# Optimization experiments

Measured on AMD Instinct MI355X. Metric: run time of the kernel, lower is better.

The kernel has to match this reference:

```python
import jax, jax.numpy as jnp
import numpy as np

B, N, F, K = 512, 512, 512, 10
D = F // 2

def setup_inputs() -> dict:
    key = jax.random.key(0)
    k1, k2, k3 = jax.random.split(key, 3)
    ins_emb = jax.random.normal(k1, (B, N, F), dtype=jnp.float32)
    attn = jax.random.uniform(k2, (B, N, 1), dtype=jnp.float32)
    # xavier_uniform for a (D, D) linear weight
    limit = float(np.sqrt(6.0 / (D + D)))
    W = jax.random.uniform(k3, (D, D), dtype=jnp.float32, minval=-limit, maxval=limit)
    return {"ins_emb": ins_emb, "attn": attn, "W": W}

def reference(ins_emb, attn, W):
    d = ins_emb.shape[-1] // 2
    drug = ins_emb[:, :, :d]          # [B, N, d]
    dis = ins_emb[:, :, d:]           # [B, N, d]
    # torch Linear: drug @ W^T, then per-instance dot with dis -> scalar
    proj = jnp.einsum('bnd,ed->bne', drug, W)          # [B, N, d]
    pred = jnp.sum(proj * dis, axis=-1, keepdims=True) # [B, N, 1]
    attn_pred = attn * pred                            # [B, N, 1]
    topk_vals, _ = jax.lax.top_k(attn_pred[:, :, 0], K)  # [B, K]
    return jnp.mean(topk_vals, axis=1, keepdims=True)    # [B, 1]
```

## Files before the change

### kernel.cpp

```cpp
#include <hip/hip_runtime.h>
#include <hip/hip_bf16.h>
#include <cstdint>

#define BB 512
#define NN 512
#define FF 512
#define DD 256
#define KTOP 10
#define BM 32
#define GRID 256
#define TPB 32

typedef __attribute__((ext_vector_type(8))) short bf16x8;
typedef __attribute__((ext_vector_type(4))) float f32x4;

__device__ __forceinline__ ushort f2bf(float x){
  union { __hip_bfloat16 h; ushort u; } cv;
  cv.h = __float2bfloat16(x);
  return cv.u;
}

__device__ __forceinline__ bf16x8 cvt8(f32x4 a, f32x4 b){
  bf16x8 r;
  r[0]=(short)f2bf(a[0]); r[1]=(short)f2bf(a[1]); r[2]=(short)f2bf(a[2]); r[3]=(short)f2bf(a[3]);
  r[4]=(short)f2bf(b[0]); r[5]=(short)f2bf(b[1]); r[6]=(short)f2bf(b[2]); r[7]=(short)f2bf(b[3]);
  return r;
}

#define GL2LDS(GSRC, LDST)                                                          \
  __builtin_amdgcn_global_load_lds(                                                 \
      (const __attribute__((address_space(1))) uint32_t*)(uintptr_t)(GSRC),         \
      (__attribute__((address_space(3))) uint32_t*)(uint32_t)(uintptr_t)(LDST),     \
      16, 0, 0)

__global__ __launch_bounds__(512, 2)
void fused_kernel(const float* __restrict__ emb, const float* __restrict__ attn,
                  const float* __restrict__ W, float* __restrict__ out){
  __shared__ float LA[BM*FF];
  __shared__ float LB[BM*FF];
  __shared__ float red[2][8][BM];
  __shared__ float attn_l[TPB*BM];
  __shared__ float scores_l[TPB*BM];

  const int tid  = threadIdx.x;
  const int w    = tid >> 6;
  const int lane = tid & 63;
  const int g    = lane >> 4;
  const int c    = lane & 15;
  const int s    = w & 3;
  const int h    = w >> 2;

  int offs[8];
#pragma unroll
  for (int i = 0; i < 8; ++i){
    int idx = w*8 + i;
    int r = idx >> 1, hf = idx & 1;
    offs[i] = r*FF + hf*256 + ((lane ^ (r & 7)) << 2);
  }
  const float* tbase = emb + (size_t)blockIdx.x * (TPB*BM*FF);

#pragma unroll
  for (int i = 0; i < 8; ++i)
    GL2LDS(tbase + offs[i], &LA[(w*8 + i)*256]);

  attn_l[tid]       = attn[blockIdx.x*(TPB*BM) + tid];
  attn_l[tid + 512] = attn[blockIdx.x*(TPB*BM) + 512 + tid];

  bf16x8 Wf[4][4];
#pragma unroll
  for (int eb = 0; eb < 4; ++eb)
#pragma unroll
    for (int kb = 0; kb < 4; ++kb){
      const float* wp = W + (s*64 + eb*16 + c)*DD + h*128 + kb*32 + g*8;
      f32x4 q0 = *reinterpret_cast<const f32x4*>(wp);
      f32x4 q1 = *reinterpret_cast<const f32x4*>(wp + 4);
      Wf[eb][kb] = cvt8(q0, q1);
    }

  __syncthreads();

#define TILE_BODY(T, RD, WR, PAR)                                                   \
  do {                                                                              \
    if ((T) + 1 < TPB){                                                             \
      const float* nb_ = tbase + (size_t)((T)+1) * (BM*FF);                         \
      _Pragma("unroll")                                                             \
      for (int i = 0; i < 8; ++i)                                                   \
        GL2LDS(nb_ + offs[i], &WR[(w*8 + i)*256]);                                  \
    }                                                                               \
    const f32x4* Lv = (const f32x4*)&RD[0];                                         \
    _Pragma("unroll")                                                               \
    for (int mb = 0; mb < 2; ++mb){                                                 \
      const int m0 = mb*16;                                                         \
      const int rb = (m0 + c)*128;                                                  \
      const int x  = c & 7;                                                         \
      bf16x8 af[4];                                                                 \
      _Pragma("unroll")                                                             \
      for (int kb = 0; kb < 4; ++kb){                                               \
        int ch0 = h*32 + kb*8 + g*2;                                                \
        f32x4 q0 = Lv[rb + ((ch0    ) ^ x)];                                        \
        f32x4 q1 = Lv[rb + ((ch0 + 1) ^ x)];                                        \
        af[kb] = cvt8(q0, q1);                                                      \
      }                                                                             \
      float rs0=0.f, rs1=0.f, rs2=0.f, rs3=0.f;                                     \
      _Pragma("unroll")                                                             \
      for (int eb = 0; eb < 4; ++eb){                                               \
        f32x4 acc = {0.f, 0.f, 0.f, 0.f};                                           \
        _Pragma("unroll")                                                           \
        for (int kb = 0; kb < 4; ++kb)                                              \
          acc = __builtin_amdgcn_mfma_f32_16x16x32_bf16(af[kb], Wf[eb][kb], acc, 0, 0, 0); \
        const int sb = 64 + s*16 + eb*4 + (c >> 2);                                 \
        const int e3 = c & 3;                                                       \
        _Pragma("unroll")                                                           \
        for (int j = 0; j < 4; ++j){                                                \
          const int row = m0 + g*4 + j;                                             \
          const int fi  = row*FF + ((sb ^ (row & 7)) << 2) + e3;                    \
          float d = RD[fi];                                                         \
          if      (j == 0) rs0 += acc[0]*d;                                         \
          else if (j == 1) rs1 += acc[1]*d;                                         \
          else if (j == 2) rs2 += acc[2]*d;                                         \
          else             rs3 += acc[3]*d;                                         \
        }                                                                           \
      }                                                                             \
      rs0 += __shfl_xor(rs0,1); rs0 += __shfl_xor(rs0,2); rs0 += __shfl_xor(rs0,4); rs0 += __shfl_xor(rs0,8); \
      rs1 += __shfl_xor(rs1,1); rs1 += __shfl_xor(rs1,2); rs1 += __shfl_xor(rs1,4); rs1 += __shfl_xor(rs1,8); \
      rs2 += __shfl_xor(rs2,1); rs2 += __shfl_xor(rs2,2); rs2 += __shfl_xor(rs2,4); rs2 += __shfl_xor(rs2,8); \
      rs3 += __shfl_xor(rs3,1); rs3 += __shfl_xor(rs3,2); rs3 += __shfl_xor(rs3,4); rs3 += __shfl_xor(rs3,8); \
      if (c == 0){                                                                  \
        red[PAR][w][m0 + g*4 + 0] = rs0;                                            \
        red[PAR][w][m0 + g*4 + 1] = rs1;                                            \
        red[PAR][w][m0 + g*4 + 2] = rs2;                                            \
        red[PAR][w][m0 + g*4 + 3] = rs3;                                            \
      }                                                                             \
    }                                                                               \
    __syncthreads();                       \
    if (tid < BM){                                                                  \
      float sum = red[PAR][0][tid] + red[PAR][1][tid] + red[PAR][2][tid] + red[PAR][3][tid] \
                + red[PAR][4][tid] + red[PAR][5][tid] + red[PAR][6][tid] + red[PAR][7][tid]; \
      scores_l[(T)*BM + tid] = attn_l[(T)*BM + tid] * sum;                          \
    }                                                                               \
  } while(0)

  for (int t = 0; t < TPB; t += 2){
    TILE_BODY(t,     LA, LB, 0);
    TILE_BODY(t + 1, LB, LA, 1);
  }
#undef TILE_BODY

  __syncthreads();

  if (w < 2){
    const float* sc = scores_l + w*NN;
    float v0,v1,v2,v3,v4,v5,v6,v7;
    v0=sc[lane];     v1=sc[64+lane];  v2=sc[128+lane]; v3=sc[192+lane];
    v4=sc[256+lane]; v5=sc[320+lane]; v6=sc[384+lane]; v7=sc[448+lane];
    float total = 0.f;
    for (int it = 0; it < KTOP; ++it){
      float m = v0; int mj = 0;
      if (v1>m){m=v1;mj=1;} if (v2>m){m=v2;mj=2;} if (v3>m){m=v3;mj=3;}
      if (v4>m){m=v4;mj=4;} if (v5>m){m=v5;mj=5;} if (v6>m){m=v6;mj=6;}
      if (v7>m){m=v7;mj=7;}
      float bm = m; int bl = lane;
#pragma unroll
      for (int off = 32; off; off >>= 1){
        float om = __shfl_xor(bm, off);
        int   ol = __shfl_xor(bl, off);
        if (om > bm || (om == bm && ol < bl)){ bm = om; bl = ol; }
      }
      total += bm;
      if (lane == bl){
        if (mj==0) v0=-3.0e38f; else if (mj==1) v1=-3.0e38f;
        else if (mj==2) v2=-3.0e38f; else if (mj==3) v3=-3.0e38f;
        else if (mj==4) v4=-3.0e38f; else if (mj==5) v5=-3.0e38f;
        else if (mj==6) v6=-3.0e38f; else v7=-3.0e38f;
      }
    }
    if (lane == 0) out[blockIdx.x*2 + w] = total * (1.0f / KTOP);
  }
}

extern "C" void kernel_launch(void* const* d_in, const int* in_sizes, int n_in,
                              void* d_out, int out_size, void* d_ws, size_t ws_size,
                              hipStream_t stream){
  const float* emb  = (const float*)d_in[0];
  const float* attn = (const float*)d_in[1];
  const float* W    = (const float*)d_in[2];
  float* out = (float*)d_out;

  fused_kernel<<<GRID, 512, 0, stream>>>(emb, attn, W, out);
}
```

Before: 107.6 us.

## Use one 256-thread block per batch with 16-row tiles over 512 blocks

The kernel now launches 512 blocks of 256 threads, one per batch element, instead of 256 blocks of 512 threads that each covered two batches. Tiles shrink to 16 rows, and each wave handles 8 output column blocks, holding W fragments for 128 output columns in registers. The goal is to double the number of blocks so more CUs are busy and to halve LDS per block so more blocks fit per CU. The cost is twice the W-fragment registers per thread, which puts pressure on occupancy, and a barrier every 16 rows instead of every 32.

```diff
diff --git a/kernel.cpp b/kernel.cpp
--- a/kernel.cpp
+++ b/kernel.cpp
@@ -7,8 +7,8 @@
 #define FF 512
 #define DD 256
 #define KTOP 10
-#define BM 32
-#define GRID 256
+#define BM 16
+#define GRID 512
 #define TPB 32
 
 typedef __attribute__((ext_vector_type(8))) short bf16x8;
@@ -33,22 +33,22 @@
       (__attribute__((address_space(3))) uint32_t*)(uint32_t)(uintptr_t)(LDST),     \
       16, 0, 0)
 
-__global__ __launch_bounds__(512, 2)
+__global__ __launch_bounds__(256, 2)
 void fused_kernel(const float* __restrict__ emb, const float* __restrict__ attn,
                   const float* __restrict__ W, float* __restrict__ out){
   __shared__ float LA[BM*FF];
   __shared__ float LB[BM*FF];
-  __shared__ float red[2][8][BM];
-  __shared__ float attn_l[TPB*BM];
-  __shared__ float scores_l[TPB*BM];
+  __shared__ float red[2][4][BM];
+  __shared__ float attn_l[NN];
+  __shared__ float scores_l[NN];
 
   const int tid  = threadIdx.x;
   const int w    = tid >> 6;
   const int lane = tid & 63;
   const int g    = lane >> 4;
   const int c    = lane & 15;
-  const int s    = w & 3;
-  const int h    = w >> 2;
+  const int s    = w & 1;
+  const int h    = w >> 1;
 
   int offs[8];
 #pragma unroll
@@ -57,21 +57,21 @@
     int r = idx >> 1, hf = idx & 1;
     offs[i] = r*FF + hf*256 + ((lane ^ (r & 7)) << 2);
   }
-  const float* tbase = emb + (size_t)blockIdx.x * (TPB*BM*FF);
+  const float* tbase = emb + (size_t)blockIdx.x * (NN*FF);
 
 #pragma unroll
   for (int i = 0; i < 8; ++i)
     GL2LDS(tbase + offs[i], &LA[(w*8 + i)*256]);
 
-  attn_l[tid]       = attn[blockIdx.x*(TPB*BM) + tid];
-  attn_l[tid + 512] = attn[blockIdx.x*(TPB*BM) + 512 + tid];
+  attn_l[tid]       = attn[blockIdx.x*NN + tid];
+  attn_l[tid + 256] = attn[blockIdx.x*NN + 256 + tid];
 
-  bf16x8 Wf[4][4];
+  bf16x8 Wf[8][4];
 #pragma unroll
-  for (int eb = 0; eb < 4; ++eb)
+  for (int eb = 0; eb < 8; ++eb)
 #pragma unroll
     for (int kb = 0; kb < 4; ++kb){
-      const float* wp = W + (s*64 + eb*16 + c)*DD + h*128 + kb*32 + g*8;
+      const float* wp = W + (s*128 + eb*16 + c)*DD + h*128 + kb*32 + g*8;
       f32x4 q0 = *reinterpret_cast<const f32x4*>(wp);
       f32x4 q1 = *reinterpret_cast<const f32x4*>(wp + 4);
       Wf[eb][kb] = cvt8(q0, q1);
@@ -88,54 +88,50 @@
         GL2LDS(nb_ + offs[i], &WR[(w*8 + i)*256]);                                  \
     }                                                                               \
     const f32x4* Lv = (const f32x4*)&RD[0];                                         \
+    const int rb = c*128;                                                           \
+    const int x  = c & 7;                                                           \
+    bf16x8 af[4];                                                                   \
     _Pragma("unroll")                                                               \
-    for (int mb = 0; mb < 2; ++mb){                                                 \
-      const int m0 = mb*16;                                                         \
-      const int rb = (m0 + c)*128;                                                  \
-      const int x  = c & 7;                                                         \
-      bf16x8 af[4];                                                                 \
+    for (int kb = 0; kb < 4; ++kb){                                                 \
+      int ch0 = h*32 + kb*8 + g*2;                                                  \
+      f32x4 q0 = Lv[rb + ((ch0    ) ^ x)];                                          \
+      f32x4 q1 = Lv[rb + ((ch0 + 1) ^ x)];                                          \
+      af[kb] = cvt8(q0, q1);                                                        \
+    }                                                                               \
+    float rs0=0.f, rs1=0.f, rs2=0.f, rs3=0.f;                                       \
+    _Pragma("unroll")                                                               \
+    for (int eb = 0; eb < 8; ++eb){                                                 \
+      f32x4 acc = {0.f, 0.f, 0.f, 0.f};                                             \
       _Pragma("unroll")                                                             \
-      for (int kb = 0; kb < 4; ++kb){                                               \
-        int ch0 = h*32 + kb*8 + g*2;                                                \
-        f32x4 q0 = Lv[rb + ((ch0    ) ^ x)];                                        \
-        f32x4 q1 = Lv[rb + ((ch0 + 1) ^ x)];                                        \
-        af[kb] = cvt8(q0, q1);                                                      \
+      for (int kb = 0; kb < 4; ++kb)                                                \
+        acc = __builtin_amdgcn_mfma_f32_16x16x32_bf16(af[kb], Wf[eb][kb], acc, 0, 0, 0); \
+      const int sb = 64 + s*32 + eb*4 + (c >> 2);                                   \
+      const int e3 = c & 3;                                                         \
+      _Pragma("unroll")                                                             \
+      for (int j = 0; j < 4; ++j){                                                  \
+        const int row = g*4 + j;                                                    \
+        const int fi  = row*FF + ((sb ^ (row & 7)) << 2) + e3;                      \
+        float d = RD[fi];                                                           \
+        if      (j == 0) rs0 += acc[0]*d;                                           \
+        else if (j == 1) rs1 += acc[1]*d;                                           \
+        else if (j == 2) rs2 += acc[2]*d;                                           \
+        else             rs3 += acc[3]*d;                                           \
       }                                                                             \
-      float rs0=0.f, rs1=0.f, rs2=0.f, rs3=0.f;                                     \
-      _Pragma("unroll")                                                             \
-      for (int eb = 0; eb < 4; ++eb){                                               \
-        f32x4 acc = {0.f, 0.f, 0.f, 0.f};                                           \
-        _Pragma("unroll")                                                           \
-        for (int kb = 0; kb < 4; ++kb)                                              \
-          acc = __builtin_amdgcn_mfma_f32_16x16x32_bf16(af[kb], Wf[eb][kb], acc, 0, 0, 0); \
-        const int sb = 64 + s*16 + eb*4 + (c >> 2);                                 \
-        const int e3 = c & 3;                                                       \
-        _Pragma("unroll")                                                           \
-        for (int j = 0; j < 4; ++j){                                                \
-          const int row = m0 + g*4 + j;                                             \
-          const int fi  = row*FF + ((sb ^ (row & 7)) << 2) + e3;                    \
-          float d = RD[fi];                                                         \
-          if      (j == 0) rs0 += acc[0]*d;                                         \
-          else if (j == 1) rs1 += acc[1]*d;                                         \
-          else if (j == 2) rs2 += acc[2]*d;                                         \
-          else             rs3 += acc[3]*d;                                         \
-        }                                                                           \
-      }                                                                             \
-      rs0 += __shfl_xor(rs0,1); rs0 += __shfl_xor(rs0,2); rs0 += __shfl_xor(rs0,4); rs0 += __shfl_xor(rs0,8); \
-      rs1 += __shfl_xor(rs1,1); rs1 += __shfl_xor(rs1,2); rs1 += __shfl_xor(rs1,4); rs1 += __shfl_xor(rs1,8); \
-      rs2 += __shfl_xor(rs2,1); rs2 += __shfl_xor(rs2,2); rs2 += __shfl_xor(rs2,4); rs2 += __shfl_xor(rs2,8); \
-      rs3 += __shfl_xor(rs3,1); rs3 += __shfl_xor(rs3,2); rs3 += __shfl_xor(rs3,4); rs3 += __shfl_xor(rs3,8); \
-      if (c == 0){                                                                  \
-        red[PAR][w][m0 + g*4 + 0] = rs0;                                            \
-        red[PAR][w][m0 + g*4 + 1] = rs1;                                            \
-        red[PAR][w][m0 + g*4 + 2] = rs2;                                            \
-        red[PAR][w][m0 + g*4 + 3] = rs3;                                            \
-      }                                                                             \
+    }                                                                               \
+    rs0 += __shfl_xor(rs0,1); rs0 += __shfl_xor(rs0,2); rs0 += __shfl_xor(rs0,4); rs0 += __shfl_xor(rs0,8); \
+    rs1 += __shfl_xor(rs1,1); rs1 += __shfl_xor(rs1,2); rs1 += __shfl_xor(rs1,4); rs1 += __shfl_xor(rs1,8); \
+    rs2 += __shfl_xor(rs2,1); rs2 += __shfl_xor(rs2,2); rs2 += __shfl_xor(rs2,4); rs2 += __shfl_xor(rs2,8); \
+    rs3 += __shfl_xor(rs3,1); rs3 += __shfl_xor(rs3,2); rs3 += __shfl_xor(rs3,4); rs3 += __shfl_xor(rs3,8); \
+    if (c == 0){                                                                    \
+      red[PAR][w][g*4 + 0] = rs0;                                                   \
+      red[PAR][w][g*4 + 1] = rs1;                                                   \
+      red[PAR][w][g*4 + 2] = rs2;                                                   \
+      red[PAR][w][g*4 + 3] = rs3;                                                   \
     }                                                                               \
     __syncthreads();                       \
     if (tid < BM){                                                                  \
-      float sum = red[PAR][0][tid] + red[PAR][1][tid] + red[PAR][2][tid] + red[PAR][3][tid] \
-                + red[PAR][4][tid] + red[PAR][5][tid] + red[PAR][6][tid] + red[PAR][7][tid]; \
+      float sum = red[PAR][0][tid] + red[PAR][1][tid]                               \
+                + red[PAR][2][tid] + red[PAR][3][tid];                              \
       scores_l[(T)*BM + tid] = attn_l[(T)*BM + tid] * sum;                          \
     }                                                                               \
   } while(0)
@@ -148,11 +144,10 @@
 
   __syncthreads();
 
-  if (w < 2){
-    const float* sc = scores_l + w*NN;
+  if (w == 0){
     float v0,v1,v2,v3,v4,v5,v6,v7;
-    v0=sc[lane];     v1=sc[64+lane];  v2=sc[128+lane]; v3=sc[192+lane];
-    v4=sc[256+lane]; v5=sc[320+lane]; v6=sc[384+lane]; v7=sc[448+lane];
+    v0=scores_l[lane];     v1=scores_l[64+lane];  v2=scores_l[128+lane]; v3=scores_l[192+lane];
+    v4=scores_l[256+lane]; v5=scores_l[320+lane]; v6=scores_l[384+lane]; v7=scores_l[448+lane];
     float total = 0.f;
     for (int it = 0; it < KTOP; ++it){
       float m = v0; int mj = 0;
@@ -174,7 +169,7 @@
         else if (mj==6) v6=-3.0e38f; else v7=-3.0e38f;
       }
     }
-    if (lane == 0) out[blockIdx.x*2 + w] = total * (1.0f / KTOP);
+    if (lane == 0) out[blockIdx.x] = total * (1.0f / KTOP);
   }
 }
 
@@ -186,5 +181,5 @@
   const float* W    = (const float*)d_in[2];
   float* out = (float*)d_out;
 
-  fused_kernel<<<GRID, 512, 0, stream>>>(emb, attn, W, out);
+  fused_kernel<<<GRID, 256, 0, stream>>>(emb, attn, W, out);
 }
```

Measured after the change: 235.3 us. +118.7%, slower.
